# Kernel optimization log

Hardware: AMD Instinct MI355X
Metric: run time of the kernel (lower is better)

## Reference

```python
import jax, jax.numpy as jnp
import numpy as np


def _maxpool2x2(x):
    # x: [N, C, H, W] -> [N, C, H//2, W//2]
    return jax.lax.reduce_window(x, -jnp.inf, jax.lax.max,
                                 (1, 1, 2, 2), (1, 1, 2, 2), 'VALID')


def _head(a, W1, b1, W2, b2, W3, b3):
    # headModel: maxpool -> (adaptive avgpool to 7x7 is identity here) -> flatten -> classifier (eval mode)
    mp = _maxpool2x2(a)                      # [N, 512, 7, 7]
    flat = mp.reshape(mp.shape[0], -1)       # [N, 25088]
    h = jax.nn.relu(flat @ W1.T + b1)        # [N, 4096]
    h = jax.nn.relu(h @ W2.T + b2)           # [N, 4096]
    return h @ W3.T + b3                     # [N, 1000]


def setup_inputs() -> dict:
    key = jax.random.key(0)
    ks = jax.random.split(key, 7)
    C, HW, FC, NC = 512, 14, 4096, 1000
    acts = jax.random.uniform(ks[0], (1, C, HW, HW), dtype=jnp.float32)  # post-ReLU feature map
    s1 = 1.0 / np.sqrt(C * 7 * 7)
    s2 = 1.0 / np.sqrt(FC)
    return {
        'activations': acts,
        'W1': jax.random.normal(ks[1], (FC, C * 7 * 7), dtype=jnp.float32) * s1,
        'b1': jax.random.normal(ks[2], (FC,), dtype=jnp.float32) * 0.01,
        'W2': jax.random.normal(ks[3], (FC, FC), dtype=jnp.float32) * s2,
        'b2': jax.random.normal(ks[4], (FC,), dtype=jnp.float32) * 0.01,
        'W3': jax.random.normal(ks[5], (NC, FC), dtype=jnp.float32) * s2,
        'b3': jax.random.normal(ks[6], (NC,), dtype=jnp.float32) * 0.01,
        'ht': 224,
        'wt': 224,
    }


def reference(activations, W1, b1, W2, b2, W3, b3, ht, wt):
    C = activations.shape[1]
    logits = _head(activations, W1, b1, W2, b2, W3, b3)   # [1, 1000]
    img_class = jnp.argmax(logits[0])
    base = logits[0, img_class]

    # Batch all C channel ablations: abl[i] = activations with channel i zeroed.
    mask = (1.0 - jnp.eye(C, dtype=activations.dtype))[:, :, None, None]  # [C, C, 1, 1]
    abl = activations * mask                                              # [C, C, 14, 14]
    logits_new = _head(abl, W1, b1, W2, b2, W3, b3)                        # [C, 1000]
    alpha = (base - jnp.take(logits_new, img_class, axis=1)) / base        # [C]

    # fused = relu(sum_i alpha_i * bilinear_resize(act_i)); resize is linear,
    # so weight in activation space and do one resize (same math as the loop).
    weighted = jnp.einsum('c,chw->hw', alpha, activations[0])              # [14, 14]
    sal = jax.image.resize(weighted[None, None], (1, 1, ht, wt),
                           method='bilinear')[0, 0]                        # [ht, wt]
    fused = jax.nn.relu(sal)
    mn, mx = fused.min(), fused.max()
    denom = jnp.where(mx != mn, mx - mn, 1.0)
    fused = jnp.where(mx != mn, (fused - mn) / denom, fused)
    return fused, img_class
```

## Files before the change

### kernel.cpp

```cpp
#include <hip/hip_runtime.h>
#include <math.h>

#define CCH 512
#define F1 25088
#define FC 4096
#define NCLS 1000
#define OW 224

#define WS_DT 0
#define WS_MP (WS_DT + FC*CCH)
#define WS_H1PRE (WS_MP + F1)
#define WS_H1 (WS_H1PRE + FC)
#define WS_H2 (WS_H1 + FC)
#define WS_LOGITS (WS_H2 + FC)
#define WS_CLSBASE (WS_LOGITS + NCLS)
#define WS_LOGPART (WS_CLSBASE + 2)
#define WS_MINMAX (WS_LOGPART + 64*CCH)
#define WS_WEIGHTED (WS_MINMAX + 2)
#define WS_W2B (WS_WEIGHTED + 196)
#define WS_A (WS_W2B + FC*FC/2)
#define WS_END (WS_A + CCH*FC/2)
#define WS_NEED_BYTES ((size_t)WS_END * 4)

typedef __attribute__((ext_vector_type(8))) short bfrag;
typedef __attribute__((ext_vector_type(4))) float f32x4;

static __device__ __forceinline__ unsigned short f2bf(float x) {
    unsigned u = __float_as_uint(x);
    unsigned r = 0x7FFFu + ((u >> 16) & 1u);
    return (unsigned short)((u + r) >> 16);
}

#define GLD16(g, l) __builtin_amdgcn_global_load_lds( \
    (const __attribute__((address_space(1))) void*)(g), \
    (__attribute__((address_space(3))) void*)(l), 16, 0, 0)

__global__ void k_maxpool(const float* __restrict__ act, float* __restrict__ ws) {
    int t = threadIdx.x;
    if (blockIdx.x == 0) {
        if (t == 0) ((int*)(ws + WS_MINMAX))[0] = 0x7F800000;
        if (t == 1) ((int*)(ws + WS_MINMAX))[1] = 0;
    }
    int idx = blockIdx.x * 256 + t;
    if (idx >= CCH * 49) return;
    int c = idx / 49, r = idx % 49, y = r / 7, x = r % 7;
    const float* a = act + c * 196 + (2 * y) * 14 + 2 * x;
    float m = fmaxf(fmaxf(a[0], a[1]), fmaxf(a[14], a[15]));
    ws[WS_MP + idx] = m;
}

__global__ __launch_bounds__(256) void k_phi2(const float* __restrict__ W1,
                                              const float* __restrict__ mp,
                                              float* __restrict__ Dt) {
    __shared__ float buf[12544];
    int j = blockIdx.x, t = threadIdx.x;
    const float* row = W1 + (size_t)j * F1;
    #pragma unroll
    for (int h = 0; h < 2; ++h) {
        __syncthreads();
        const float4* src = (const float4*)(row + h * 12544);
        const float4* msc = (const float4*)(mp + h * 12544);
        for (int n = t; n < 3136; n += 256) {
            float4 w = src[n], m = msc[n];
            float4 p;
            p.x = w.x * m.x; p.y = w.y * m.y; p.z = w.z * m.z; p.w = w.w * m.w;
            *(float4*)&buf[n * 4] = p;
        }
        __syncthreads();
        const float* b = buf + t * 49;
        float s = 0.f;
        #pragma unroll
        for (int k = 0; k < 49; ++k) s += b[k];
        Dt[(size_t)j * CCH + h * 256 + t] = s;
    }
}

__global__ void k_h1(const float* __restrict__ Dt, const float* __restrict__ b1,
                     float* __restrict__ h1pre, float* __restrict__ h1) {
    int j = blockIdx.x, t = threadIdx.x;
    const float* row = Dt + (size_t)j * CCH;
    float s = 0.f;
    for (int i = t; i < CCH; i += 64) s += row[i];
    for (int off = 32; off > 0; off >>= 1) s += __shfl_down(s, off, 64);
    if (t == 0) { float v = b1[j] + s; h1pre[j] = v; h1[j] = fmaxf(v, 0.f); }
}

template <bool RELU, bool CVT>
__global__ void k_gemv4096(const float* __restrict__ M, const float* __restrict__ v,
                           const float* __restrict__ bias, float* __restrict__ out,
                           unsigned short* __restrict__ Mb) {
    int j = blockIdx.x, t = threadIdx.x;
    const float4* row = (const float4*)(M + (size_t)j * FC);
    const float4* vv = (const float4*)v;
    float s = 0.f;
    #pragma unroll
    for (int q = 0; q < 4; ++q) {
        int n = q * 256 + t;
        float4 w = row[n], x = vv[n];
        s += w.x * x.x + w.y * x.y + w.z * x.z + w.w * x.w;
        if (CVT) {
            ushort4 b;
            b.x = f2bf(w.x); b.y = f2bf(w.y); b.z = f2bf(w.z); b.w = f2bf(w.w);
            *(ushort4*)&Mb[(size_t)j * FC + n * 4] = b;
        }
    }
    __shared__ float red[256];
    red[t] = s; __syncthreads();
    if (t < 128) red[t] += red[t + 128]; __syncthreads();
    if (t < 64)  red[t] += red[t + 64];  __syncthreads();
    if (t < 64) {
        float x = red[t];
        for (int off = 32; off > 0; off >>= 1) x += __shfl_down(x, off, 64);
        if (t == 0) { float r = bias[j] + x; out[j] = RELU ? fmaxf(r, 0.f) : r; }
    }
}

__global__ void k_argmax(const float* __restrict__ logits, float* __restrict__ clsbase,
                         float* __restrict__ dout_cls) {
    int t = threadIdx.x;
    float best = -INFINITY; int bi = NCLS;
    for (int n = t; n < NCLS; n += 256) {
        float v = logits[n];
        if (v > best || (v == best && n < bi)) { best = v; bi = n; }
    }
    __shared__ float bv[256]; __shared__ int bidx[256];
    bv[t] = best; bidx[t] = bi; __syncthreads();
    for (int o = 128; o > 0; o >>= 1) {
        if (t < o) {
            float v2 = bv[t + o]; int i2 = bidx[t + o];
            if (v2 > bv[t] || (v2 == bv[t] && i2 < bidx[t])) { bv[t] = v2; bidx[t] = i2; }
        }
        __syncthreads();
    }
    if (t == 0) { clsbase[0] = (float)bidx[0]; clsbase[1] = bv[0]; *dout_cls = (float)bidx[0]; }
}

__global__ __launch_bounds__(256) void k_abuild(const float* __restrict__ Dt,
                                                const float* __restrict__ h1pre,
                                                unsigned short* __restrict__ A) {
    __shared__ unsigned short tile[64][72];
    int kt = blockIdx.x, it = blockIdx.y, t = threadIdx.x;
    int k0 = kt * 64, i0 = it * 64;
    #pragma unroll
    for (int q = 0; q < 16; ++q) {
        int kk = q * 4 + (t >> 6);
        int ii = t & 63;
        float v = fmaxf(h1pre[k0 + kk] - Dt[(size_t)(k0 + kk) * CCH + i0 + ii], 0.f);
        tile[kk][ii] = f2bf(v);
    }
    __syncthreads();
    #pragma unroll
    for (int q = 0; q < 4; ++q) {
        int c = q * 256 + t;
        int ii = c >> 4, kc = c & 15;
        ushort4 v;
        v.x = tile[kc * 4 + 0][ii]; v.y = tile[kc * 4 + 1][ii];
        v.z = tile[kc * 4 + 2][ii]; v.w = tile[kc * 4 + 3][ii];
        *(ushort4*)&A[(size_t)(i0 + ii) * FC + k0 + kc * 4] = v;
    }
}

__global__ __launch_bounds__(256) void k_mfma_abl(
    const unsigned short* __restrict__ A, const unsigned short* __restrict__ W2b,
    const float* __restrict__ b2, const float* __restrict__ W3,
    const float* __restrict__ clsbase, float* __restrict__ logit_part) {
    __shared__ char lds[16384];
    int nj = blockIdx.x;
    int mi = blockIdx.y;
    int t = threadIdx.x;
    int wid = t >> 6, lane = t & 63, lr = lane & 15, lh = lane >> 4;
    int i0 = mi * 64, j0 = nj * 64;

    const char* Ab = (const char*)(A + (size_t)i0 * FC);
    const char* Bb = (const char*)(W2b + (size_t)j0 * FC);
    char* As = lds;
    char* Bs = lds + 8192;

    int c0 = t, c1 = t + 256;
    int r0 = c0 >> 3, r1 = c1 >> 3;
    size_t goff0 = (size_t)r0 * 8192 + (size_t)(((c0 & 7) ^ (r0 & 7)) * 16);
    size_t goff1 = (size_t)r1 * 8192 + (size_t)(((c1 & 7) ^ (r1 & 7)) * 16);

    int arow = wid * 16 + lr;
    int aoff0 = arow * 128 + ((lh) ^ (arow & 7)) * 16;
    int aoff1 = arow * 128 + ((lh + 4) ^ (arow & 7)) * 16;

    f32x4 acc[4];
    #pragma unroll
    for (int jf = 0; jf < 4; ++jf) acc[jf] = (f32x4){0.f, 0.f, 0.f, 0.f};

    for (int kb = 0; kb < FC * 2; kb += 128) {
        __syncthreads();
        GLD16(Ab + goff0 + kb, As + c0 * 16);
        GLD16(Ab + goff1 + kb, As + c1 * 16);
        GLD16(Bb + goff0 + kb, Bs + c0 * 16);
        GLD16(Bb + goff1 + kb, Bs + c1 * 16);
        __syncthreads();
        bfrag a0 = *(const bfrag*)(As + aoff0);
        bfrag a1 = *(const bfrag*)(As + aoff1);
        #pragma unroll
        for (int jf = 0; jf < 4; ++jf) {
            int brow = jf * 16 + lr;
            bfrag b0 = *(const bfrag*)(Bs + brow * 128 + ((lh) ^ (brow & 7)) * 16);
            bfrag b1 = *(const bfrag*)(Bs + brow * 128 + ((lh + 4) ^ (brow & 7)) * 16);
            acc[jf] = __builtin_amdgcn_mfma_f32_16x16x32_bf16(a0, b0, acc[jf], 0, 0, 0);
            acc[jf] = __builtin_amdgcn_mfma_f32_16x16x32_bf16(a1, b1, acc[jf], 0, 0, 0);
        }
    }

    int cls = (int)clsbase[0];
    const float* w3r = W3 + (size_t)cls * FC;
    float part[4] = {0.f, 0.f, 0.f, 0.f};
    #pragma unroll
    for (int jf = 0; jf < 4; ++jf) {
        int j = j0 + jf * 16 + lr;
        float bb = b2[j], w3 = w3r[j];
        #pragma unroll
        for (int r = 0; r < 4; ++r)
            part[r] += fmaxf(acc[jf][r] + bb, 0.f) * w3;
    }
    #pragma unroll
    for (int r = 0; r < 4; ++r) {
        part[r] += __shfl_xor(part[r], 1, 64);
        part[r] += __shfl_xor(part[r], 2, 64);
        part[r] += __shfl_xor(part[r], 4, 64);
        part[r] += __shfl_xor(part[r], 8, 64);
    }
    if (lr == 0) {
        float4 v;
        v.x = part[0]; v.y = part[1]; v.z = part[2]; v.w = part[3];
        *(float4*)&logit_part[(size_t)nj * CCH + i0 + wid * 16 + lh * 4] = v;
    }
}

__global__ __launch_bounds__(256) void k_gemm_abl(
    const float* __restrict__ Dt, const float* __restrict__ h1pre,
    const float* __restrict__ W2, const float* __restrict__ b2,
    const float* __restrict__ W3, const float* __restrict__ clsbase,
    float* __restrict__ logit_part) {
    int mi = blockIdx.x, nj = blockIdx.y, t = threadIdx.x;
    int tx = t & 15, ty = t >> 4;
    int i0 = mi * 64, j0 = nj * 64;
    __shared__ float As[16][64];
    __shared__ float Bs[16][65];
    float acc[4][4] = {};
    for (int k0 = 0; k0 < FC; k0 += 16) {
        #pragma unroll
        for (int r = 0; r < 4; ++r) {
            int e = t + 256 * r; int kk = e >> 6, ii = e & 63;
            float hp = h1pre[k0 + kk];
            float d = Dt[(size_t)(k0 + kk) * CCH + i0 + ii];
            As[kk][ii] = fmaxf(hp - d, 0.f);
        }
        {
            int jj = t >> 2, kks = (t & 3) * 4;
            const float4 wv = *(const float4*)(W2 + (size_t)(j0 + jj) * FC + k0 + kks);
            Bs[kks + 0][jj] = wv.x; Bs[kks + 1][jj] = wv.y;
            Bs[kks + 2][jj] = wv.z; Bs[kks + 3][jj] = wv.w;
        }
        __syncthreads();
        #pragma unroll
        for (int kk = 0; kk < 16; ++kk) {
            float4 a4 = *(const float4*)&As[kk][tx * 4];
            float av[4] = {a4.x, a4.y, a4.z, a4.w};
            float bv[4] = {Bs[kk][ty * 4 + 0], Bs[kk][ty * 4 + 1],
                           Bs[kk][ty * 4 + 2], Bs[kk][ty * 4 + 3]};
            #pragma unroll
            for (int a = 0; a < 4; ++a)
                #pragma unroll
                for (int b = 0; b < 4; ++b)
                    acc[a][b] = fmaf(av[a], bv[b], acc[a][b]);
        }
        __syncthreads();
    }
    int cls = (int)clsbase[0];
    const float* w3r = W3 + (size_t)cls * FC;
    float part[4] = {0.f, 0.f, 0.f, 0.f};
    #pragma unroll
    for (int b = 0; b < 4; ++b) {
        int j2 = j0 + ty * 4 + b;
        float bb = b2[j2], w3 = w3r[j2];
        #pragma unroll
        for (int a = 0; a < 4; ++a) {
            float v = fmaxf(acc[a][b] + bb, 0.f);
            part[a] = fmaf(v, w3, part[a]);
        }
    }
    __shared__ float red[16][68];
    #pragma unroll
    for (int a = 0; a < 4; ++a) red[ty][tx * 4 + a] = part[a];
    __syncthreads();
    if (t < 64) {
        float s = 0.f;
        #pragma unroll
        for (int q = 0; q < 16; ++q) s += red[q][t];
        logit_part[nj * CCH + i0 + t] = s;
    }
}

__global__ void k_weighted(const float* __restrict__ logit_part, const float* __restrict__ b3,
                           const float* __restrict__ clsbase, const float* __restrict__ act,
                           float* __restrict__ weighted) {
    __shared__ float sA[CCH];
    int t = threadIdx.x;
    int cls = (int)clsbase[0]; float base = clsbase[1];
    float b3c = b3[cls];
    for (int i = t; i < CCH; i += 256) {
        float s = 0.f;
        for (int q = 0; q < 64; ++q) s += logit_part[q * CCH + i];
        float logit_i = s + b3c;
        sA[i] = (base - logit_i) / base;
    }
    __syncthreads();
    for (int p = t; p < 196; p += 256) {
        float s = 0.f;
        for (int i = 0; i < CCH; ++i) s = fmaf(sA[i], act[i * 196 + p], s);
        weighted[p] = s;
    }
}

__global__ void k_resize(const float* __restrict__ weighted, float* __restrict__ out,
                         int* __restrict__ minmax) {
    __shared__ float sW[196];
    int t = threadIdx.x;
    if (t < 196) sW[t] = weighted[t];
    __syncthreads();
    int pix = blockIdx.x * 256 + t;
    int y = pix / OW, x = pix % OW;
    float uy = (y + 0.5f) * 0.0625f - 0.5f;
    float ux = (x + 0.5f) * 0.0625f - 0.5f;
    float y0f = floorf(uy), x0f = floorf(ux);
    float fy = uy - y0f, fx = ux - x0f;
    int y0 = (int)y0f, x0 = (int)x0f;
    int y0c = min(max(y0, 0), 13), y1c = min(max(y0 + 1, 0), 13);
    int x0c = min(max(x0, 0), 13), x1c = min(max(x0 + 1, 0), 13);
    float v00 = sW[y0c * 14 + x0c], v01 = sW[y0c * 14 + x1c];
    float v10 = sW[y1c * 14 + x0c], v11 = sW[y1c * 14 + x1c];
    float v0 = v00 + (v01 - v00) * fx;
    float v1 = v10 + (v11 - v10) * fx;
    float v = v0 + (v1 - v0) * fy;
    float f = fmaxf(v, 0.f);
    out[pix] = f;
    __shared__ float rmn[256], rmx[256];
    rmn[t] = f; rmx[t] = f; __syncthreads();
    for (int o = 128; o > 0; o >>= 1) {
        if (t < o) { rmn[t] = fminf(rmn[t], rmn[t + o]); rmx[t] = fmaxf(rmx[t], rmx[t + o]); }
        __syncthreads();
    }
    if (t == 0) {
        atomicMin(&minmax[0], __float_as_int(rmn[0]));
        atomicMax(&minmax[1], __float_as_int(rmx[0]));
    }
}

__global__ void k_norm(float* __restrict__ out, const int* __restrict__ minmax) {
    float mn = __int_as_float(minmax[0]);
    float mx = __int_as_float(minmax[1]);
    int pix = blockIdx.x * 256 + threadIdx.x;
    if (mx != mn) out[pix] = (out[pix] - mn) / (mx - mn);
}

extern "C" void kernel_launch(void* const* d_in, const int* in_sizes, int n_in,
                              void* d_out, int out_size, void* d_ws, size_t ws_size,
                              hipStream_t stream) {
    const float* act = (const float*)d_in[0];
    const float* W1  = (const float*)d_in[1];
    const float* b1  = (const float*)d_in[2];
    const float* W2  = (const float*)d_in[3];
    const float* b2  = (const float*)d_in[4];
    const float* W3  = (const float*)d_in[5];
    const float* b3  = (const float*)d_in[6];
    float* out = (float*)d_out;
    float* ws = (float*)d_ws;
    const bool fast = (ws_size >= WS_NEED_BYTES);

    k_maxpool<<<98, 256, 0, stream>>>(act, ws);
    k_phi2<<<4096, 256, 0, stream>>>(W1, ws + WS_MP, ws + WS_DT);
    k_h1<<<4096, 64, 0, stream>>>(ws + WS_DT, b1, ws + WS_H1PRE, ws + WS_H1);
    if (fast) {
        k_gemv4096<true, true><<<4096, 256, 0, stream>>>(
            W2, ws + WS_H1, b2, ws + WS_H2, (unsigned short*)(ws + WS_W2B));
    } else {
        k_gemv4096<true, false><<<4096, 256, 0, stream>>>(
            W2, ws + WS_H1, b2, ws + WS_H2, nullptr);
    }
    k_gemv4096<false, false><<<1000, 256, 0, stream>>>(W3, ws + WS_H2, b3,
                                                       ws + WS_LOGITS, nullptr);
    k_argmax<<<1, 256, 0, stream>>>(ws + WS_LOGITS, ws + WS_CLSBASE, out + 50176);
    if (fast) {
        k_abuild<<<dim3(64, 8), 256, 0, stream>>>(ws + WS_DT, ws + WS_H1PRE,
                                                  (unsigned short*)(ws + WS_A));
        k_mfma_abl<<<dim3(64, 8), 256, 0, stream>>>(
            (const unsigned short*)(ws + WS_A), (const unsigned short*)(ws + WS_W2B),
            b2, W3, ws + WS_CLSBASE, ws + WS_LOGPART);
    } else {
        k_gemm_abl<<<dim3(8, 64), 256, 0, stream>>>(ws + WS_DT, ws + WS_H1PRE, W2, b2, W3,
                                                    ws + WS_CLSBASE, ws + WS_LOGPART);
    }
    k_weighted<<<1, 256, 0, stream>>>(ws + WS_LOGPART, b3, ws + WS_CLSBASE, act,
                                      ws + WS_WEIGHTED);
    k_resize<<<196, 256, 0, stream>>>(ws + WS_WEIGHTED, out, (int*)(ws + WS_MINMAX));
    k_norm<<<196, 256, 0, stream>>>(out, (const int*)(ws + WS_MINMAX));
}
```

Measured before the change: 241.3 us.

## Restructure ablation GEMM into split-K MFMA tiles with inline W2 bf16 conversion

```diff
diff --git a/kernel.cpp b/kernel.cpp
--- a/kernel.cpp
+++ b/kernel.cpp
@@ -6,20 +6,25 @@
 #define FC 4096
 #define NCLS 1000
 #define OW 224
+#define KSPLIT 4
+#define KSLICE 1024
+#define PSTRIDE (CCH*FC)
 
 #define WS_DT 0
 #define WS_MP (WS_DT + FC*CCH)
-#define WS_H1PRE (WS_MP + F1)
+#define WS_QS (WS_MP + F1)
+#define WS_H1PRE (WS_QS + FC*4)
 #define WS_H1 (WS_H1PRE + FC)
 #define WS_H2 (WS_H1 + FC)
 #define WS_LOGITS (WS_H2 + FC)
 #define WS_CLSBASE (WS_LOGITS + NCLS)
-#define WS_LOGPART (WS_CLSBASE + 2)
-#define WS_MINMAX (WS_LOGPART + 64*CCH)
+#define WS_ALPHA (WS_CLSBASE + 2)
+#define WS_MINMAX (WS_ALPHA + CCH)
 #define WS_WEIGHTED (WS_MINMAX + 2)
-#define WS_W2B (WS_WEIGHTED + 196)
-#define WS_A (WS_W2B + FC*FC/2)
-#define WS_END (WS_A + CCH*FC/2)
+#define WS_LOGPART (WS_WEIGHTED + 196)
+#define WS_A (WS_LOGPART + 64*CCH)
+#define WS_PART (WS_A + CCH*FC/2)
+#define WS_END (WS_PART + KSPLIT*CCH*FC)
 #define WS_NEED_BYTES ((size_t)WS_END * 4)
 
 typedef __attribute__((ext_vector_type(8))) short bfrag;
@@ -49,46 +54,53 @@
     ws[WS_MP + idx] = m;
 }
 
-__global__ __launch_bounds__(256) void k_phi2(const float* __restrict__ W1,
+__global__ __launch_bounds__(256) void k_phi3(const float* __restrict__ W1,
                                               const float* __restrict__ mp,
-                                              float* __restrict__ Dt) {
-    __shared__ float buf[12544];
-    int j = blockIdx.x, t = threadIdx.x;
-    const float* row = W1 + (size_t)j * F1;
-    #pragma unroll
-    for (int h = 0; h < 2; ++h) {
-        __syncthreads();
-        const float4* src = (const float4*)(row + h * 12544);
-        const float4* msc = (const float4*)(mp + h * 12544);
-        for (int n = t; n < 3136; n += 256) {
-            float4 w = src[n], m = msc[n];
-            float4 p;
-            p.x = w.x * m.x; p.y = w.y * m.y; p.z = w.z * m.z; p.w = w.w * m.w;
-            *(float4*)&buf[n * 4] = p;
-        }
-        __syncthreads();
-        const float* b = buf + t * 49;
+                                              float* __restrict__ Dt,
+                                              float* __restrict__ qs) {
+    __shared__ float buf[6272];
+    __shared__ float red[128];
+    int b = blockIdx.x;
+    int j = b >> 2, q = b & 3;
+    int t = threadIdx.x;
+    const float4* src = (const float4*)(W1 + (size_t)j * F1 + q * 6272);
+    const float4* msc = (const float4*)(mp + q * 6272);
+    for (int n = t; n < 1568; n += 256) {
+        float4 w = src[n], m = msc[n];
+        float4 p;
+        p.x = w.x * m.x; p.y = w.y * m.y; p.z = w.z * m.z; p.w = w.w * m.w;
+        *(float4*)&buf[n * 4] = p;
+    }
+    __syncthreads();
+    if (t < 128) {
+        const float* bb = buf + t * 49;
         float s = 0.f;
         #pragma unroll
-        for (int k = 0; k < 49; ++k) s += b[k];
-        Dt[(size_t)j * CCH + h * 256 + t] = s;
-    }
-}
-
-__global__ void k_h1(const float* __restrict__ Dt, const float* __restrict__ b1,
-                     float* __restrict__ h1pre, float* __restrict__ h1) {
-    int j = blockIdx.x, t = threadIdx.x;
-    const float* row = Dt + (size_t)j * CCH;
-    float s = 0.f;
-    for (int i = t; i < CCH; i += 64) s += row[i];
-    for (int off = 32; off > 0; off >>= 1) s += __shfl_down(s, off, 64);
-    if (t == 0) { float v = b1[j] + s; h1pre[j] = v; h1[j] = fmaxf(v, 0.f); }
-}
-
-template <bool RELU, bool CVT>
+        for (int k = 0; k < 49; ++k) s += bb[k];
+        Dt[(size_t)j * CCH + q * 128 + t] = s;
+        red[t] = s;
+    }
+    __syncthreads();
+    if (t < 64) {
+        float v = red[t] + red[t + 64];
+        for (int off = 32; off > 0; off >>= 1) v += __shfl_down(v, off, 64);
+        if (t == 0) qs[b] = v;
+    }
+}
+
+__global__ void k_h1b(const float* __restrict__ qs, const float* __restrict__ b1,
+                      float* __restrict__ h1pre, float* __restrict__ h1) {
+    int j = blockIdx.x * 256 + threadIdx.x;
+    if (j < FC) {
+        const float* g = qs + j * 4;
+        float v = b1[j] + ((g[0] + g[1]) + (g[2] + g[3]));
+        h1pre[j] = v; h1[j] = fmaxf(v, 0.f);
+    }
+}
+
+template <bool RELU>
 __global__ void k_gemv4096(const float* __restrict__ M, const float* __restrict__ v,
-                           const float* __restrict__ bias, float* __restrict__ out,
-                           unsigned short* __restrict__ Mb) {
+                           const float* __restrict__ bias, float* __restrict__ out) {
     int j = blockIdx.x, t = threadIdx.x;
     const float4* row = (const float4*)(M + (size_t)j * FC);
     const float4* vv = (const float4*)v;
@@ -98,11 +110,6 @@
         int n = q * 256 + t;
         float4 w = row[n], x = vv[n];
         s += w.x * x.x + w.y * x.y + w.z * x.z + w.w * x.w;
-        if (CVT) {
-            ushort4 b;
-            b.x = f2bf(w.x); b.y = f2bf(w.y); b.z = f2bf(w.z); b.w = f2bf(w.w);
-            *(ushort4*)&Mb[(size_t)j * FC + n * 4] = b;
-        }
     }
     __shared__ float red[256];
     red[t] = s; __syncthreads();
@@ -160,76 +167,118 @@
     }
 }
 
-__global__ __launch_bounds__(256) void k_mfma_abl(
-    const unsigned short* __restrict__ A, const unsigned short* __restrict__ W2b,
-    const float* __restrict__ b2, const float* __restrict__ W3,
-    const float* __restrict__ clsbase, float* __restrict__ logit_part) {
-    __shared__ char lds[16384];
+__global__ __launch_bounds__(512) void k_mfma_all(
+    const unsigned short* __restrict__ A, const float* __restrict__ W2,
+    float* __restrict__ part) {
+    __shared__ char As[65536];
+    __shared__ char Bs[8192];
     int nj = blockIdx.x;
-    int mi = blockIdx.y;
+    int ks = blockIdx.y;
     int t = threadIdx.x;
     int wid = t >> 6, lane = t & 63, lr = lane & 15, lh = lane >> 4;
-    int i0 = mi * 64, j0 = nj * 64;
-
-    const char* Ab = (const char*)(A + (size_t)i0 * FC);
-    const char* Bb = (const char*)(W2b + (size_t)j0 * FC);
-    char* As = lds;
-    char* Bs = lds + 8192;
-
-    int c0 = t, c1 = t + 256;
-    int r0 = c0 >> 3, r1 = c1 >> 3;
-    size_t goff0 = (size_t)r0 * 8192 + (size_t)(((c0 & 7) ^ (r0 & 7)) * 16);
-    size_t goff1 = (size_t)r1 * 8192 + (size_t)(((c1 & 7) ^ (r1 & 7)) * 16);
-
-    int arow = wid * 16 + lr;
-    int aoff0 = arow * 128 + ((lh) ^ (arow & 7)) * 16;
-    int aoff1 = arow * 128 + ((lh + 4) ^ (arow & 7)) * 16;
-
-    f32x4 acc[4];
-    #pragma unroll
-    for (int jf = 0; jf < 4; ++jf) acc[jf] = (f32x4){0.f, 0.f, 0.f, 0.f};
-
-    for (int kb = 0; kb < FC * 2; kb += 128) {
-        __syncthreads();
-        GLD16(Ab + goff0 + kb, As + c0 * 16);
-        GLD16(Ab + goff1 + kb, As + c1 * 16);
-        GLD16(Bb + goff0 + kb, Bs + c0 * 16);
-        GLD16(Bb + goff1 + kb, Bs + c1 * 16);
-        __syncthreads();
-        bfrag a0 = *(const bfrag*)(As + aoff0);
-        bfrag a1 = *(const bfrag*)(As + aoff1);
-        #pragma unroll
-        for (int jf = 0; jf < 4; ++jf) {
-            int brow = jf * 16 + lr;
-            bfrag b0 = *(const bfrag*)(Bs + brow * 128 + ((lh) ^ (brow & 7)) * 16);
-            bfrag b1 = *(const bfrag*)(Bs + brow * 128 + ((lh + 4) ^ (brow & 7)) * 16);
-            acc[jf] = __builtin_amdgcn_mfma_f32_16x16x32_bf16(a0, b0, acc[jf], 0, 0, 0);
-            acc[jf] = __builtin_amdgcn_mfma_f32_16x16x32_bf16(a1, b1, acc[jf], 0, 0, 0);
-        }
-    }
-
-    int cls = (int)clsbase[0];
+    int j0 = nj * 64;
+
+    int wrow = t >> 3, wch = t & 7;
+    const float* wsrc = W2 + (size_t)(j0 + wrow) * FC + (size_t)ks * KSLICE + wch * 8;
+    char* bdst = Bs + ((size_t)wrow * 8 + (wch ^ (wrow & 7))) * 16;
+
+    f32x4 acc[4][4];
+    #pragma unroll
+    for (int f = 0; f < 4; ++f)
+        #pragma unroll
+        for (int n = 0; n < 4; ++n) acc[f][n] = (f32x4){0.f, 0.f, 0.f, 0.f};
+
+    for (int kst = 0; kst < KSLICE; kst += 64) {
+        size_t k0 = (size_t)ks * KSLICE + kst;
+        __syncthreads();
+        #pragma unroll
+        for (int r = 0; r < 8; ++r) {
+            int c = t + 512 * r;
+            int row = c >> 3, ch = c & 7;
+            size_t g = (size_t)row * FC + k0 + (size_t)((ch ^ (row & 7)) * 8);
+            GLD16(A + g, As + (size_t)c * 16);
+        }
+        {
+            const float4 wa = ((const float4*)(wsrc + kst))[0];
+            const float4 wb = ((const float4*)(wsrc + kst))[1];
+            union { bfrag v; unsigned short u[8]; } pk;
+            pk.u[0] = f2bf(wa.x); pk.u[1] = f2bf(wa.y);
+            pk.u[2] = f2bf(wa.z); pk.u[3] = f2bf(wa.w);
+            pk.u[4] = f2bf(wb.x); pk.u[5] = f2bf(wb.y);
+            pk.u[6] = f2bf(wb.z); pk.u[7] = f2bf(wb.w);
+            *(bfrag*)bdst = pk.v;
+        }
+        __syncthreads();
+        #pragma unroll
+        for (int kf = 0; kf < 2; ++kf) {
+            bfrag bfr[4];
+            #pragma unroll
+            for (int n = 0; n < 4; ++n) {
+                int brow = n * 16 + lr;
+                bfr[n] = *(const bfrag*)(Bs + ((size_t)brow * 8 + ((kf * 4 + lh) ^ (brow & 7))) * 16);
+            }
+            #pragma unroll
+            for (int f = 0; f < 4; ++f) {
+                int arow = wid * 64 + f * 16 + lr;
+                bfrag af = *(const bfrag*)(As + ((size_t)arow * 8 + ((kf * 4 + lh) ^ (arow & 7))) * 16);
+                #pragma unroll
+                for (int n = 0; n < 4; ++n)
+                    acc[f][n] = __builtin_amdgcn_mfma_f32_16x16x32_bf16(af, bfr[n], acc[f][n], 0, 0, 0);
+            }
+        }
+    }
+    float* base = part + (size_t)ks * PSTRIDE;
+    #pragma unroll
+    for (int f = 0; f < 4; ++f) {
+        #pragma unroll
+        for (int n = 0; n < 4; ++n) {
+            #pragma unroll
+            for (int r = 0; r < 4; ++r) {
+                int row = wid * 64 + f * 16 + lh * 4 + r;
+                base[(size_t)row * FC + j0 + n * 16 + lr] = acc[f][n][r];
+            }
+        }
+    }
+}
+
+__global__ __launch_bounds__(256) void k_alpha(
+    const float* __restrict__ part, const float* __restrict__ b2,
+    const float* __restrict__ W3, const float* __restrict__ b3,
+    const float* __restrict__ clsbase, float* __restrict__ alpha) {
+    int i = blockIdx.x, t = threadIdx.x;
+    int cls = (int)clsbase[0]; float base = clsbase[1];
     const float* w3r = W3 + (size_t)cls * FC;
-    float part[4] = {0.f, 0.f, 0.f, 0.f};
-    #pragma unroll
-    for (int jf = 0; jf < 4; ++jf) {
-        int j = j0 + jf * 16 + lr;
-        float bb = b2[j], w3 = w3r[j];
-        #pragma unroll
-        for (int r = 0; r < 4; ++r)
-            part[r] += fmaxf(acc[jf][r] + bb, 0.f) * w3;
-    }
-    #pragma unroll
-    for (int r = 0; r < 4; ++r) {
-        part[r] += __shfl_xor(part[r], 1, 64);
-        part[r] += __shfl_xor(part[r], 2, 64);
-        part[r] += __shfl_xor(part[r], 4, 64);
-        part[r] += __shfl_xor(part[r], 8, 64);
-    }
-    if (lr == 0) {
-        float4 v;
-        v.x = part[0]; v.y = part[1]; v.z = part[2]; v.w = part[3];
-        *(float4*)&logit_part[(size_t)nj * CCH + i0 + wid * 16 + lh * 4] = v;
+    const float* p0 = part + (size_t)i * FC;
+    float s = 0.f;
+    for (int j = t; j < FC; j += 256) {
+        float v = ((p0[j] + p0[j + PSTRIDE]) + (p0[j + 2 * PSTRIDE] + p0[j + 3 * PSTRIDE]))
+                  + b2[j];
+        s += fmaxf(v, 0.f) * w3r[j];
+    }
+    __shared__ float red[256];
+    red[t] = s; __syncthreads();
+    if (t < 128) red[t] += red[t + 128]; __syncthreads();
+    if (t < 64)  red[t] += red[t + 64];  __syncthreads();
+    if (t < 64) {
+        float x = red[t];
+        for (int off = 32; off > 0; off >>= 1) x += __shfl_down(x, off, 64);
+        if (t == 0) {
+            float logit = x + b3[cls];
+            alpha[i] = (base - logit) / base;
+        }
+    }
+}
+
+__global__ void k_weighted2(const float* __restrict__ alpha, const float* __restrict__ act,
+                            float* __restrict__ weighted) {
+    __shared__ float sA[CCH];
+    int t = threadIdx.x;
+    for (int i = t; i < CCH; i += 256) sA[i] = alpha[i];
+    __syncthreads();
+    for (int p = t; p < 196; p += 256) {
+        float s = 0.f;
+        for (int i = 0; i < CCH; ++i) s = fmaf(sA[i], act[i * 196 + p], s);
+        weighted[p] = s;
     }
 }
 
@@ -241,30 +290,28 @@
     int mi = blockIdx.x, nj = blockIdx.y, t = threadIdx.x;
     int tx = t & 15, ty = t >> 4;
     int i0 = mi * 64, j0 = nj * 64;
-    __shared__ float As[16][64];
-    __shared__ float Bs[16][65];
+    __shared__ float As2[16][64];
+    __shared__ float Bs2[16][65];
     float acc[4][4] = {};
     for (int k0 = 0; k0 < FC; k0 += 16) {
         #pragma unroll
         for (int r = 0; r < 4; ++r) {
             int e = t + 256 * r; int kk = e >> 6, ii = e & 63;
-            float hp = h1pre[k0 + kk];
-            float d = Dt[(size_t)(k0 + kk) * CCH + i0 + ii];
-            As[kk][ii] = fmaxf(hp - d, 0.f);
+            As2[kk][ii] = fmaxf(h1pre[k0 + kk] - Dt[(size_t)(k0 + kk) * CCH + i0 + ii], 0.f);
         }
         {
             int jj = t >> 2, kks = (t & 3) * 4;
             const float4 wv = *(const float4*)(W2 + (size_t)(j0 + jj) * FC + k0 + kks);
-            Bs[kks + 0][jj] = wv.x; Bs[kks + 1][jj] = wv.y;
-            Bs[kks + 2][jj] = wv.z; Bs[kks + 3][jj] = wv.w;
+            Bs2[kks + 0][jj] = wv.x; Bs2[kks + 1][jj] = wv.y;
+            Bs2[kks + 2][jj] = wv.z; Bs2[kks + 3][jj] = wv.w;
         }
         __syncthreads();
         #pragma unroll
         for (int kk = 0; kk < 16; ++kk) {
-            float4 a4 = *(const float4*)&As[kk][tx * 4];
+            float4 a4 = *(const float4*)&As2[kk][tx * 4];
             float av[4] = {a4.x, a4.y, a4.z, a4.w};
-            float bv[4] = {Bs[kk][ty * 4 + 0], Bs[kk][ty * 4 + 1],
-                           Bs[kk][ty * 4 + 2], Bs[kk][ty * 4 + 3]};
+            float bv[4] = {Bs2[kk][ty * 4 + 0], Bs2[kk][ty * 4 + 1],
+                           Bs2[kk][ty * 4 + 2], Bs2[kk][ty * 4 + 3]};
             #pragma unroll
             for (int a = 0; a < 4; ++a)
                 #pragma unroll
@@ -275,48 +322,34 @@
     }
     int cls = (int)clsbase[0];
     const float* w3r = W3 + (size_t)cls * FC;
-    float part[4] = {0.f, 0.f, 0.f, 0.f};
+    float prt[4] = {0.f, 0.f, 0.f, 0.f};
     #pragma unroll
     for (int b = 0; b < 4; ++b) {
         int j2 = j0 + ty * 4 + b;
         float bb = b2[j2], w3 = w3r[j2];
         #pragma unroll
-        for (int a = 0; a < 4; ++a) {
-            float v = fmaxf(acc[a][b] + bb, 0.f);
-            part[a] = fmaf(v, w3, part[a]);
-        }
-    }
-    __shared__ float red[16][68];
-    #pragma unroll
-    for (int a = 0; a < 4; ++a) red[ty][tx * 4 + a] = part[a];
+        for (int a = 0; a < 4; ++a) prt[a] = fmaf(fmaxf(acc[a][b] + bb, 0.f), w3, prt[a]);
+    }
+    __shared__ float red2[16][68];
+    #pragma unroll
+    for (int a = 0; a < 4; ++a) red2[ty][tx * 4 + a] = prt[a];
     __syncthreads();
     if (t < 64) {
         float s = 0.f;
         #pragma unroll
-        for (int q = 0; q < 16; ++q) s += red[q][t];
+        for (int q = 0; q < 16; ++q) s += red2[q][t];
         logit_part[nj * CCH + i0 + t] = s;
     }
 }
 
-__global__ void k_weighted(const float* __restrict__ logit_part, const float* __restrict__ b3,
-                           const float* __restrict__ clsbase, const float* __restrict__ act,
-                           float* __restrict__ weighted) {
-    __shared__ float sA[CCH];
-    int t = threadIdx.x;
+__global__ void k_alpha_fb(const float* __restrict__ logit_part, const float* __restrict__ b3,
+                           const float* __restrict__ clsbase, float* __restrict__ alpha) {
+    int t = blockIdx.x * 256 + threadIdx.x;
+    if (t >= CCH) return;
     int cls = (int)clsbase[0]; float base = clsbase[1];
-    float b3c = b3[cls];
-    for (int i = t; i < CCH; i += 256) {
-        float s = 0.f;
-        for (int q = 0; q < 64; ++q) s += logit_part[q * CCH + i];
-        float logit_i = s + b3c;
-        sA[i] = (base - logit_i) / base;
-    }
-    __syncthreads();
-    for (int p = t; p < 196; p += 256) {
-        float s = 0.f;
-        for (int i = 0; i < CCH; ++i) s = fmaf(sA[i], act[i * 196 + p], s);
-        weighted[p] = s;
-    }
+    float s = 0.f;
+    for (int q = 0; q < 64; ++q) s += logit_part[q * CCH + t];
+    alpha[t] = (base - (s + b3[cls])) / base;
 }
 
 __global__ void k_resize(const float* __restrict__ weighted, float* __restrict__ out,
@@ -375,30 +408,25 @@
     const bool fast = (ws_size >= WS_NEED_BYTES);
 
     k_maxpool<<<98, 256, 0, stream>>>(act, ws);
-    k_phi2<<<4096, 256, 0, stream>>>(W1, ws + WS_MP, ws + WS_DT);
-    k_h1<<<4096, 64, 0, stream>>>(ws + WS_DT, b1, ws + WS_H1PRE, ws + WS_H1);
-    if (fast) {
-        k_gemv4096<true, true><<<4096, 256, 0, stream>>>(
-            W2, ws + WS_H1, b2, ws + WS_H2, (unsigned short*)(ws + WS_W2B));
-    } else {
-        k_gemv4096<true, false><<<4096, 256, 0, stream>>>(
-            W2, ws + WS_H1, b2, ws + WS_H2, nullptr);
-    }
-    k_gemv4096<false, false><<<1000, 256, 0, stream>>>(W3, ws + WS_H2, b3,
-                                                       ws + WS_LOGITS, nullptr);
+    k_phi3<<<16384, 256, 0, stream>>>(W1, ws + WS_MP, ws + WS_DT, ws + WS_QS);
+    k_h1b<<<16, 256, 0, stream>>>(ws + WS_QS, b1, ws + WS_H1PRE, ws + WS_H1);
+    k_gemv4096<true><<<4096, 256, 0, stream>>>(W2, ws + WS_H1, b2, ws + WS_H2);
+    k_gemv4096<false><<<1000, 256, 0, stream>>>(W3, ws + WS_H2, b3, ws + WS_LOGITS);
     k_argmax<<<1, 256, 0, stream>>>(ws + WS_LOGITS, ws + WS_CLSBASE, out + 50176);
     if (fast) {
         k_abuild<<<dim3(64, 8), 256, 0, stream>>>(ws + WS_DT, ws + WS_H1PRE,
                                                   (unsigned short*)(ws + WS_A));
-        k_mfma_abl<<<dim3(64, 8), 256, 0, stream>>>(
-            (const unsigned short*)(ws + WS_A), (const unsigned short*)(ws + WS_W2B),
-            b2, W3, ws + WS_CLSBASE, ws + WS_LOGPART);
+        k_mfma_all<<<dim3(64, KSPLIT), 512, 0, stream>>>(
+            (const unsigned short*)(ws + WS_A), W2, ws + WS_PART);
+        k_alpha<<<CCH, 256, 0, stream>>>(ws + WS_PART, b2, W3, b3,
+                                         ws + WS_CLSBASE, ws + WS_ALPHA);
     } else {
         k_gemm_abl<<<dim3(8, 64), 256, 0, stream>>>(ws + WS_DT, ws + WS_H1PRE, W2, b2, W3,
                                                     ws + WS_CLSBASE, ws + WS_LOGPART);
-    }
-    k_weighted<<<1, 256, 0, stream>>>(ws + WS_LOGPART, b3, ws + WS_CLSBASE, act,
-                                      ws + WS_WEIGHTED);
+        k_alpha_fb<<<2, 256, 0, stream>>>(ws + WS_LOGPART, b3, ws + WS_CLSBASE,
+                                          ws + WS_ALPHA);
+    }
+    k_weighted2<<<1, 256, 0, stream>>>(ws + WS_ALPHA, act, ws + WS_WEIGHTED);
     k_resize<<<196, 256, 0, stream>>>(ws + WS_WEIGHTED, out, (int*)(ws + WS_MINMAX));
     k_norm<<<196, 256, 0, stream>>>(out, (const int*)(ws + WS_MINMAX));
 }
```

Measured after the change: 219.1 us. -9.2%, faster.
